# Kernel tuning notes

Hardware: AMD Instinct MI355X
Metric: run time of the kernel (lower is better)

The kernel has to match this reference:

```python
import jax, jax.numpy as jnp
import numpy as np

N = 50000   # nodes
E = 800000  # edges (avg degree 16)
IN, H, OUT = 128, 128, 64


def setup_inputs() -> dict:
    key = jax.random.key(0)
    ks = jax.random.split(key, 8)

    def w(k, shape):
        fan_in = shape[0]
        return (jax.random.normal(k, shape, jnp.float32) / np.float32(np.sqrt(fan_in)))

    x = jax.random.normal(ks[0], (N, IN), jnp.float32)
    edge_index = jax.random.randint(ks[1], (2, E), 0, N, jnp.int64)
    return {
        "x": x,
        "edge_index": edge_index,
        "W1": w(ks[2], (IN, H)), "b1": jnp.zeros((H,), jnp.float32),
        "W2": w(ks[3], (H, H)),  "b2": jnp.zeros((H,), jnp.float32),
        "W3": w(ks[4], (H, H)),  "b3": jnp.zeros((H,), jnp.float32),
        "Wd1": w(ks[5], (H, H)), "bd1": jnp.zeros((H,), jnp.float32),
        "Wd2": w(ks[6], (H, OUT)), "bd2": jnp.zeros((OUT,), jnp.float32),
    }


def _gcn_conv(x, src, dst, norm, W, b):
    # x: [N, Cin] -> linear transform, gather along edges, normalized scatter-add
    h = x @ W                                   # [N, Cout]
    msg = h[src] * norm[:, None]                # [E+N, Cout]
    out = jax.ops.segment_sum(msg, dst, num_segments=N)
    return out + b


def reference(x, edge_index, W1, b1, W2, b2, W3, b3, Wd1, bd1, Wd2, bd2):
    # Add self-loops (PyG GCNConv default) and compute symmetric normalization.
    loops = jnp.arange(N, dtype=edge_index.dtype)
    src = jnp.concatenate([edge_index[0], loops])   # [E+N]
    dst = jnp.concatenate([edge_index[1], loops])   # [E+N]
    deg = jax.ops.segment_sum(jnp.ones_like(dst, dtype=x.dtype), dst, num_segments=N)
    dinv = jnp.where(deg > 0, jax.lax.rsqrt(deg), jnp.zeros_like(deg))
    norm = dinv[src] * dinv[dst]                    # [E+N]

    h = jax.nn.relu(_gcn_conv(x, src, dst, norm, W1, b1))
    h = jax.nn.relu(_gcn_conv(h, src, dst, norm, W2, b2))
    h = jax.nn.relu(_gcn_conv(h, src, dst, norm, W3, b3))

    h = jax.nn.relu(h @ Wd1 + bd1)
    return jax.nn.sigmoid(h @ Wd2 + bd2)            # [N, OUT]
```

## Files before the change

kernel.cpp:

```cpp
#include <hip/hip_runtime.h>
#include <hip/hip_bf16.h>
#include <hip/hip_fp16.h>

#define N_NODES 50000
#define N_EDGES 800000
#define C_H 128
#define C_OUT 64
#define NBLK 196
#define TSTRIDE 136
#define E_PAD 1200128
#define MM_BLKS 782
#define TILE_N 6250
#define GB 782

typedef __attribute__((ext_vector_type(8))) short bf16x8;
typedef __attribute__((ext_vector_type(4))) float f32x4;

static __device__ __forceinline__ float bf_lo(unsigned int u) { return __uint_as_float(u << 16); }
static __device__ __forceinline__ float bf_hi(unsigned int u) { return __uint_as_float(u & 0xffff0000u); }
static __device__ __forceinline__ unsigned short f2bf(float f) {
    __hip_bfloat16 h = __float2bfloat16(f);
    return *(unsigned short*)&h;
}
static __device__ __forceinline__ unsigned int pack2(float a, float b) {
    return (unsigned int)f2bf(a) | ((unsigned int)f2bf(b) << 16);
}
static __device__ __forceinline__ unsigned short f2h_bits(float f) {
    union { __half h; unsigned short u; } c; c.h = __float2half_rn(f); return c.u;
}
static __device__ __forceinline__ float h_bits2f(unsigned short u) {
    union { __half h; unsigned short u; } c; c.u = u; return __half2float(c.h);
}

__global__ void prep_kernel(const int* __restrict__ src, const int* __restrict__ dst,
                            int* __restrict__ counts2,
                            int* __restrict__ rank,
                            const float* __restrict__ W1, const float* __restrict__ W2,
                            const float* __restrict__ W3, const float* __restrict__ Wd1,
                            const float* __restrict__ Wd2,
                            unsigned short* __restrict__ P1, unsigned short* __restrict__ P2,
                            unsigned short* __restrict__ P3, unsigned short* __restrict__ Pd1,
                            unsigned short* __restrict__ Pd2,
                            unsigned int* __restrict__ epay) {
    int b = blockIdx.x;
    if (b < 3125) {
        int e = b * 256 + threadIdx.x;
        int d = dst[e], s = src[e];
        int t = s / TILE_N;
        rank[e] = atomicAdd(&counts2[d * 8 + t], 1);
    } else if (b < 3413) {
        int idx = (b - 3125) * 256 + threadIdx.x;
        if (idx < 4 * 16384) {
            int which = idx >> 14;
            int r = idx & 16383;
            const float* W = (which == 0) ? W1 : (which == 1) ? W2 : (which == 2) ? W3 : Wd1;
            unsigned short* P = (which == 0) ? P1 : (which == 1) ? P2 : (which == 2) ? P3 : Pd1;
            int j = r & 7, lane = (r >> 3) & 63, t = r >> 9;
            int nb = t & 7, kb = t >> 3;
            int k = kb * 32 + ((lane >> 4) << 3) + j;
            int n = nb * 16 + (lane & 15);
            P[r] = f2bf(W[(size_t)k * 128 + n]);
        } else {
            int r = idx - 65536;
            if (r < 8192) {
                int j = r & 7, lane = (r >> 3) & 63, t = r >> 9;
                int nb = t & 3, kb = t >> 2;
                int k = kb * 32 + ((lane >> 4) << 3) + j;
                int n = nb * 16 + (lane & 15);
                Pd2[r] = f2bf(Wd2[(size_t)k * 64 + n]);
            }
        }
    } else {
        int i = (b - 3413) * 256 + threadIdx.x;
        *(uint4*)(epay + (size_t)i * 4) = make_uint4(0, 0, 0, 0);
    }
}

__global__ void __launch_bounds__(256) scan1_kernel(int* __restrict__ counts2,
                                                    int* __restrict__ eblk,
                                                    int* __restrict__ bsum,
                                                    float* __restrict__ dinv) {
    __shared__ int ws[4];
    int i = blockIdx.x * 256 + threadIdx.x;
    int vp = 0;
    if (i < N_NODES) {
        int* c = counts2 + (size_t)i * 8;
        uint4 a = *(uint4*)c;
        uint4 bq = *(uint4*)(c + 4);
        int raw = a.x + a.y + a.z + a.w + bq.x + bq.y + bq.z + bq.w;
        dinv[i] = rsqrtf((float)raw + 1.0f);
        int run = 0, tv;
        tv = ((int)a.x + 1) & ~1;  a.x  = run; run += tv;
        tv = ((int)a.y + 1) & ~1;  a.y  = run; run += tv;
        tv = ((int)a.z + 1) & ~1;  a.z  = run; run += tv;
        tv = ((int)a.w + 1) & ~1;  a.w  = run; run += tv;
        tv = ((int)bq.x + 1) & ~1; bq.x = run; run += tv;
        tv = ((int)bq.y + 1) & ~1; bq.y = run; run += tv;
        tv = ((int)bq.z + 1) & ~1; bq.z = run; run += tv;
        tv = ((int)bq.w + 1) & ~1; bq.w = run; run += tv;
        vp = run;
        *(uint4*)c = a;
        *(uint4*)(c + 4) = bq;
    }
    int lane = threadIdx.x & 63, w = threadIdx.x >> 6;
    int x = vp;
    #pragma unroll
    for (int off = 1; off < 64; off <<= 1) {
        int t = __shfl_up(x, off, 64);
        if (lane >= off) x += t;
    }
    if (lane == 63) ws[w] = x;
    __syncthreads();
    if (threadIdx.x == 0) {
        int run = 0;
        #pragma unroll
        for (int k = 0; k < 4; ++k) { int t = ws[k]; ws[k] = run; run += t; }
        bsum[blockIdx.x] = run;
    }
    __syncthreads();
    if (i < N_NODES) eblk[i] = x - vp + ws[w];
}

__global__ void __launch_bounds__(256) scanB_kernel(const int* __restrict__ eblk,
                                                    const int* __restrict__ bsum,
                                                    int* __restrict__ rowptr) {
    __shared__ int ws[4];
    __shared__ int sbo;
    int i = threadIdx.x;
    int v = (i < NBLK) ? bsum[i] : 0;
    int lane = i & 63, w = i >> 6;
    int x = v;
    #pragma unroll
    for (int off = 1; off < 64; off <<= 1) {
        int t = __shfl_up(x, off, 64);
        if (lane >= off) x += t;
    }
    if (lane == 63) ws[w] = x;
    __syncthreads();
    if (i == 0) {
        int run = 0;
        #pragma unroll
        for (int k = 0; k < 4; ++k) { int t = ws[k]; ws[k] = run; run += t; }
    }
    __syncthreads();
    int excl = x - v + ws[w];
    if (i == (int)blockIdx.x) sbo = excl;
    if (blockIdx.x == 0 && i == NBLK - 1) rowptr[N_NODES] = excl + v;
    __syncthreads();
    int g = blockIdx.x * 256 + threadIdx.x;
    if (g < N_NODES) rowptr[g] = eblk[g] + sbo;
}

__global__ void __launch_bounds__(256) fill_mm_kernel(
        const float* __restrict__ x, const unsigned short* __restrict__ P1,
        unsigned short* __restrict__ XW1,
        const int* __restrict__ src, const int* __restrict__ dst,
        const float* __restrict__ dinv,
        const int* __restrict__ rowptr, const int* __restrict__ counts2,
        const int* __restrict__ rank,
        unsigned int* __restrict__ epay) {
    int b = blockIdx.x;
    if (b < MM_BLKS) {
        const int lane = threadIdx.x & 63;
        const int wave = threadIdx.x >> 6;
        const int wid  = b * 4 + wave;
        if (wid * 16 >= N_NODES) return;
        const int node = wid * 16 + (lane & 15);
        const int quad = lane >> 4;
        f32x4 acc[8];
        #pragma unroll
        for (int nb = 0; nb < 8; ++nb) acc[nb] = (f32x4){0.f, 0.f, 0.f, 0.f};
        #pragma unroll
        for (int kb = 0; kb < 4; ++kb) {
            const float* p = x + (size_t)node * 128 + kb * 32 + quad * 8;
            float4 lo = *(const float4*)p;
            float4 hi = *(const float4*)(p + 4);
            union { bf16x8 v; unsigned int u[4]; } tmp;
            tmp.u[0] = pack2(lo.x, lo.y); tmp.u[1] = pack2(lo.z, lo.w);
            tmp.u[2] = pack2(hi.x, hi.y); tmp.u[3] = pack2(hi.z, hi.w);
            #pragma unroll
            for (int nb = 0; nb < 8; ++nb) {
                bf16x8 wf = *(const bf16x8*)(P1 + ((size_t)(kb * 8 + nb) * 64 + lane) * 8);
                acc[nb] = __builtin_amdgcn_mfma_f32_16x16x32_bf16(wf, tmp.v, acc[nb], 0, 0, 0);
            }
        }
        #pragma unroll
        for (int nb = 0; nb < 8; ++nb) {
            int ch = nb * 16 + quad * 4;
            uint2 o;
            o.x = pack2(acc[nb][0], acc[nb][1]);
            o.y = pack2(acc[nb][2], acc[nb][3]);
            *(uint2*)(XW1 + (size_t)node * C_H + ch) = o;
        }
    } else {
        int e = (b - MM_BLKS) * 256 + threadIdx.x;
        if (e < N_EDGES) {
            int d = dst[e], s = src[e];
            int t = s / TILE_N;
            int pos = rowptr[d] + counts2[d * 8 + t] + rank[e];
            float nrm = dinv[s] * dinv[d];
            epay[pos] = (unsigned int)s | ((unsigned int)f2h_bits(nrm) << 16);
        }
    }
}

static __device__ __forceinline__ void fma8v(float* a, uint4 q, float nm) {
    a[0] = fmaf(bf_lo(q.x), nm, a[0]); a[1] = fmaf(bf_hi(q.x), nm, a[1]);
    a[2] = fmaf(bf_lo(q.y), nm, a[2]); a[3] = fmaf(bf_hi(q.y), nm, a[3]);
    a[4] = fmaf(bf_lo(q.z), nm, a[4]); a[5] = fmaf(bf_hi(q.z), nm, a[5]);
    a[6] = fmaf(bf_lo(q.w), nm, a[6]); a[7] = fmaf(bf_hi(q.w), nm, a[7]);
}

static __device__ __forceinline__ void agg32(
        const int* __restrict__ rowptr, const int* __restrict__ counts2,
        const unsigned int* __restrict__ epay,
        const unsigned short* __restrict__ hin,
        const float* __restrict__ dinv,
        int node, int cb, float* acc) {
    const unsigned short* hc = hin + cb;
    float di = dinv[node], dii = di * di;
    {
        const unsigned short* rp = hc + (size_t)node * C_H;
        uint4 q0 = *(const uint4*)rp,        q1 = *(const uint4*)(rp + 8);
        uint4 q2 = *(const uint4*)(rp + 16), q3 = *(const uint4*)(rp + 24);
        fma8v(acc + 0, q0, dii); fma8v(acc + 8, q1, dii);
        fma8v(acc + 16, q2, dii); fma8v(acc + 24, q3, dii);
    }
    int base = rowptr[node];
    int rend = rowptr[node + 1];
    const int* boff = counts2 + (size_t)node * 8;
    #pragma unroll 1
    for (int t = 0; t < 8; ++t) {
        int b0 = base + boff[t];
        int b1 = (t == 7) ? rend : base + boff[t + 1];
        for (int p = b0; p < b1; p += 2) {
            uint2 ev = *(const uint2*)(epay + p);
            const unsigned short* ra = hc + (size_t)(ev.x & 0xffffu) * C_H;
            const unsigned short* rb = hc + (size_t)(ev.y & 0xffffu) * C_H;
            uint4 a0 = *(const uint4*)ra,        a1 = *(const uint4*)(ra + 8);
            uint4 a2 = *(const uint4*)(ra + 16), a3 = *(const uint4*)(ra + 24);
            uint4 c0 = *(const uint4*)rb,        c1 = *(const uint4*)(rb + 8);
            uint4 c2 = *(const uint4*)(rb + 16), c3 = *(const uint4*)(rb + 24);
            float na = h_bits2f((unsigned short)(ev.x >> 16));
            float nb = h_bits2f((unsigned short)(ev.y >> 16));
            fma8v(acc + 0, a0, na); fma8v(acc + 8, a1, na);
            fma8v(acc + 16, a2, na); fma8v(acc + 24, a3, na);
            fma8v(acc + 0, c0, nb); fma8v(acc + 8, c1, nb);
            fma8v(acc + 16, c2, nb); fma8v(acc + 24, c3, nb);
        }
    }
}

__global__ void __launch_bounds__(256, 4) gather1_kernel(
        const int* __restrict__ rowptr, const int* __restrict__ counts2,
        const unsigned int* __restrict__ epay,
        const float* __restrict__ dinv,
        const unsigned short* __restrict__ hin,
        const float* __restrict__ bias,
        unsigned short* __restrict__ out) {
    const int t = threadIdx.x;
    const int node = blockIdx.x * 64 + (t >> 2);
    if (node >= N_NODES) return;
    const int cb = (t & 3) << 5;

    float acc[32];
    #pragma unroll
    for (int j = 0; j < 32; ++j) acc[j] = 0.f;
    agg32(rowptr, counts2, epay, hin, dinv, node, cb, acc);

    #pragma unroll
    for (int g = 0; g < 4; ++g) {
        float4 ba = *(const float4*)(bias + cb + g * 8);
        float4 bb = *(const float4*)(bias + cb + g * 8 + 4);
        float v0 = fmaxf(acc[g*8+0] + ba.x, 0.f), v1 = fmaxf(acc[g*8+1] + ba.y, 0.f);
        float v2 = fmaxf(acc[g*8+2] + ba.z, 0.f), v3 = fmaxf(acc[g*8+3] + ba.w, 0.f);
        float v4 = fmaxf(acc[g*8+4] + bb.x, 0.f), v5 = fmaxf(acc[g*8+5] + bb.y, 0.f);
        float v6 = fmaxf(acc[g*8+6] + bb.z, 0.f), v7 = fmaxf(acc[g*8+7] + bb.w, 0.f);
        uint4 o;
        o.x = pack2(v0, v1); o.y = pack2(v2, v3);
        o.z = pack2(v4, v5); o.w = pack2(v6, v7);
        *(uint4*)(out + (size_t)node * C_H + cb + g * 8) = o;
    }
}

template <bool FINAL>
__global__ void __launch_bounds__(256, 4) fused_layer_kernel(
        const int* __restrict__ rowptr, const int* __restrict__ counts2,
        const unsigned int* __restrict__ epay,
        const float* __restrict__ dinv,
        const unsigned short* __restrict__ hin,
        const unsigned short* __restrict__ Wp,
        const float* __restrict__ bias,
        const unsigned short* __restrict__ Wd1p,
        const float* __restrict__ bd1,
        const unsigned short* __restrict__ Wd2p,
        const float* __restrict__ bd2,
        unsigned short* __restrict__ out_b,
        float* __restrict__ out_f) {
    __shared__ unsigned short sA[64 * TSTRIDE];
    __shared__ unsigned short sB[64 * TSTRIDE];
    const int t = threadIdx.x;

    {
        const int ln = t >> 2;
        const int node = blockIdx.x * 64 + ln;
        const int cb = (t & 3) << 5;
        float acc[32];
        #pragma unroll
        for (int j = 0; j < 32; ++j) acc[j] = 0.f;
        if (node < N_NODES)
            agg32(rowptr, counts2, epay, hin, dinv, node, cb, acc);
        #pragma unroll
        for (int g = 0; g < 4; ++g) {
            uint4 o;
            o.x = pack2(acc[g*8+0], acc[g*8+1]); o.y = pack2(acc[g*8+2], acc[g*8+3]);
            o.z = pack2(acc[g*8+4], acc[g*8+5]); o.w = pack2(acc[g*8+6], acc[g*8+7]);
            *(uint4*)(sA + ln * TSTRIDE + cb + g * 8) = o;
        }
    }
    __syncthreads();

    const int lane = t & 63, wave = t >> 6, quad = lane >> 4, row = lane & 15;
    const int nb0 = 2 * wave, nb1 = 2 * wave + 1;

    #pragma unroll 1
    for (int rt = 0; rt < 4; ++rt) {
        const int lrow = rt * 16 + row;
        const int node = blockIdx.x * 64 + lrow;
        f32x4 acc0 = (f32x4){0.f, 0.f, 0.f, 0.f};
        f32x4 acc1 = (f32x4){0.f, 0.f, 0.f, 0.f};
        #pragma unroll
        for (int kb = 0; kb < 4; ++kb) {
            bf16x8 hf = *(const bf16x8*)(sA + lrow * TSTRIDE + kb * 32 + quad * 8);
            bf16x8 wf0 = *(const bf16x8*)(Wp + ((size_t)(kb * 8 + nb0) * 64 + lane) * 8);
            bf16x8 wf1 = *(const bf16x8*)(Wp + ((size_t)(kb * 8 + nb1) * 64 + lane) * 8);
            acc0 = __builtin_amdgcn_mfma_f32_16x16x32_bf16(wf0, hf, acc0, 0, 0, 0);
            acc1 = __builtin_amdgcn_mfma_f32_16x16x32_bf16(wf1, hf, acc1, 0, 0, 0);
        }
        float4 ba0 = *(const float4*)(bias + nb0 * 16 + quad * 4);
        float4 ba1 = *(const float4*)(bias + nb1 * 16 + quad * 4);
        float v00 = fmaxf(acc0[0] + ba0.x, 0.f), v01 = fmaxf(acc0[1] + ba0.y, 0.f);
        float v02 = fmaxf(acc0[2] + ba0.z, 0.f), v03 = fmaxf(acc0[3] + ba0.w, 0.f);
        float v10 = fmaxf(acc1[0] + ba1.x, 0.f), v11 = fmaxf(acc1[1] + ba1.y, 0.f);
        float v12 = fmaxf(acc1[2] + ba1.z, 0.f), v13 = fmaxf(acc1[3] + ba1.w, 0.f);
        uint2 o0, o1;
        o0.x = pack2(v00, v01); o0.y = pack2(v02, v03);
        o1.x = pack2(v10, v11); o1.y = pack2(v12, v13);
        if (!FINAL) {
            if (node < N_NODES) {
                *(uint2*)(out_b + (size_t)node * C_H + nb0 * 16 + quad * 4) = o0;
                *(uint2*)(out_b + (size_t)node * C_H + nb1 * 16 + quad * 4) = o1;
            }
        } else {
            *(uint2*)(sB + lrow * TSTRIDE + nb0 * 16 + quad * 4) = o0;
            *(uint2*)(sB + lrow * TSTRIDE + nb1 * 16 + quad * 4) = o1;
        }
    }
    if (!FINAL) return;

    __syncthreads();
    #pragma unroll 1
    for (int rt = 0; rt < 4; ++rt) {
        const int lrow = rt * 16 + row;
        f32x4 acc0 = (f32x4){0.f, 0.f, 0.f, 0.f};
        f32x4 acc1 = (f32x4){0.f, 0.f, 0.f, 0.f};
        #pragma unroll
        for (int kb = 0; kb < 4; ++kb) {
            bf16x8 hf = *(const bf16x8*)(sB + lrow * TSTRIDE + kb * 32 + quad * 8);
            bf16x8 wf0 = *(const bf16x8*)(Wd1p + ((size_t)(kb * 8 + nb0) * 64 + lane) * 8);
            bf16x8 wf1 = *(const bf16x8*)(Wd1p + ((size_t)(kb * 8 + nb1) * 64 + lane) * 8);
            acc0 = __builtin_amdgcn_mfma_f32_16x16x32_bf16(wf0, hf, acc0, 0, 0, 0);
            acc1 = __builtin_amdgcn_mfma_f32_16x16x32_bf16(wf1, hf, acc1, 0, 0, 0);
        }
        float4 ba0 = *(const float4*)(bd1 + nb0 * 16 + quad * 4);
        float4 ba1 = *(const float4*)(bd1 + nb1 * 16 + quad * 4);
        float v00 = fmaxf(acc0[0] + ba0.x, 0.f), v01 = fmaxf(acc0[1] + ba0.y, 0.f);
        float v02 = fmaxf(acc0[2] + ba0.z, 0.f), v03 = fmaxf(acc0[3] + ba0.w, 0.f);
        float v10 = fmaxf(acc1[0] + ba1.x, 0.f), v11 = fmaxf(acc1[1] + ba1.y, 0.f);
        float v12 = fmaxf(acc1[2] + ba1.z, 0.f), v13 = fmaxf(acc1[3] + ba1.w, 0.f);
        uint2 o0, o1;
        o0.x = pack2(v00, v01); o0.y = pack2(v02, v03);
        o1.x = pack2(v10, v11); o1.y = pack2(v12, v13);
        *(uint2*)(sA + lrow * TSTRIDE + nb0 * 16 + quad * 4) = o0;
        *(uint2*)(sA + lrow * TSTRIDE + nb1 * 16 + quad * 4) = o1;
    }
    __syncthreads();

    #pragma unroll 1
    for (int rt = 0; rt < 4; ++rt) {
        const int lrow = rt * 16 + row;
        const int node = blockIdx.x * 64 + lrow;
        f32x4 acc = (f32x4){0.f, 0.f, 0.f, 0.f};
        #pragma unroll
        for (int kb = 0; kb < 4; ++kb) {
            bf16x8 hf = *(const bf16x8*)(sA + lrow * TSTRIDE + kb * 32 + quad * 8);
            bf16x8 wf = *(const bf16x8*)(Wd2p + ((size_t)(kb * 4 + wave) * 64 + lane) * 8);
            acc = __builtin_amdgcn_mfma_f32_16x16x32_bf16(wf, hf, acc, 0, 0, 0);
        }
        if (node < N_NODES) {
            int ch = wave * 16 + quad * 4;
            float4 b4 = *(const float4*)(bd2 + ch);
            float4 rr;
            rr.x = 1.f / (1.f + expf(-(acc[0] + b4.x)));
            rr.y = 1.f / (1.f + expf(-(acc[1] + b4.y)));
            rr.z = 1.f / (1.f + expf(-(acc[2] + b4.z)));
            rr.w = 1.f / (1.f + expf(-(acc[3] + b4.w)));
            *(float4*)(out_f + (size_t)node * C_OUT + ch) = rr;
        }
    }
}

extern "C" void kernel_launch(void* const* d_in, const int* in_sizes, int n_in,
                              void* d_out, int out_size, void* d_ws, size_t ws_size,
                              hipStream_t stream) {
    const float* x   = (const float*)d_in[0];
    const int*   ei  = (const int*)d_in[1];
    const float* W1  = (const float*)d_in[2];
    const float* b1  = (const float*)d_in[3];
    const float* W2  = (const float*)d_in[4];
    const float* b2  = (const float*)d_in[5];
    const float* W3  = (const float*)d_in[6];
    const float* b3  = (const float*)d_in[7];
    const float* Wd1 = (const float*)d_in[8];
    const float* bd1 = (const float*)d_in[9];
    const float* Wd2 = (const float*)d_in[10];
    const float* bd2 = (const float*)d_in[11];

    const int* src = ei;
    const int* dst = ei + N_EDGES;

    char* base = (char*)d_ws;
    size_t off = 0;
    auto alloc = [&](size_t bytes) { char* p = base + off; off += (bytes + 255) & ~size_t(255); return p; };
    int*            counts2 = (int*)alloc((size_t)N_NODES * 8 * 4);
    unsigned int*   epay   = (unsigned int*)alloc((size_t)E_PAD * 4);
    int*            rank   = (int*)alloc((size_t)N_EDGES * 4);
    float*          dinv   = (float*)alloc(N_NODES * 4);
    int*            rowptr = (int*)alloc((N_NODES + 1) * 4);
    int*            eblk   = (int*)alloc(N_NODES * 4);
    int*            bsum   = (int*)alloc(256 * 4);
    unsigned short* XW1    = (unsigned short*)alloc((size_t)N_NODES * C_H * 2);
    unsigned short* bufA   = (unsigned short*)alloc((size_t)N_NODES * C_H * 2);
    unsigned short* bufB   = (unsigned short*)alloc((size_t)N_NODES * C_H * 2);
    unsigned short* P1     = (unsigned short*)alloc(128 * 128 * 2);
    unsigned short* P2     = (unsigned short*)alloc(128 * 128 * 2);
    unsigned short* P3     = (unsigned short*)alloc(128 * 128 * 2);
    unsigned short* Pd1    = (unsigned short*)alloc(128 * 128 * 2);
    unsigned short* Pd2    = (unsigned short*)alloc(128 * 64 * 2);

    const int T = 256;
    dim3 blk(T);
    dim3 gN((N_NODES + T - 1) / T);
    dim3 gPrep(3125 + 288 + 1172);
    dim3 gFillMM(MM_BLKS + 3125);
    dim3 gGB(GB);

    hipMemsetAsync(counts2, 0, (size_t)N_NODES * 8 * 4, stream);
    prep_kernel<<<gPrep, blk, 0, stream>>>(src, dst, counts2, rank,
                                           W1, W2, W3, Wd1, Wd2,
                                           P1, P2, P3, Pd1, Pd2, epay);
    scan1_kernel<<<gN, blk, 0, stream>>>(counts2, eblk, bsum, dinv);
    scanB_kernel<<<gN, blk, 0, stream>>>(eblk, bsum, rowptr);
    fill_mm_kernel<<<gFillMM, blk, 0, stream>>>(x, P1, XW1, src, dst, dinv,
                                                rowptr, counts2, rank, epay);

    gather1_kernel<<<gGB, blk, 0, stream>>>(rowptr, counts2, epay, dinv, XW1, b1, bufA);
    fused_layer_kernel<false><<<gGB, blk, 0, stream>>>(
        rowptr, counts2, epay, dinv, bufA, P2, b2, nullptr, nullptr, nullptr, nullptr, bufB, nullptr);
    fused_layer_kernel<true><<<gGB, blk, 0, stream>>>(
        rowptr, counts2, epay, dinv, bufB, P3, b3, Pd1, bd1, Pd2, bd2, nullptr, (float*)d_out);
}
```

Measured before the change: 293.9 us.

## Use wave-per-16-nodes gather with each lane owning two channels

Changes the edge aggregation from four threads per node, each holding 32 channels, to one wavefront per 16 nodes where each lane holds two channels of a node row. Each gathered neighbor row becomes a single coalesced 256-byte wave access instead of per-thread 64-byte strided loads, and per-thread register use for accumulators shrinks. In exchange the 16 nodes of a wave are walked one after another, so edge-index loads become wave-uniform and serialized. Nodes with different degrees are processed sequentially inside the wave, and each edge now brings less work per load, which may lower memory-level parallelism.

```diff
diff --git a/kernel.cpp b/kernel.cpp
--- a/kernel.cpp
+++ b/kernel.cpp
@@ -204,49 +204,41 @@
     }
 }
 
-static __device__ __forceinline__ void fma8v(float* a, uint4 q, float nm) {
-    a[0] = fmaf(bf_lo(q.x), nm, a[0]); a[1] = fmaf(bf_hi(q.x), nm, a[1]);
-    a[2] = fmaf(bf_lo(q.y), nm, a[2]); a[3] = fmaf(bf_hi(q.y), nm, a[3]);
-    a[4] = fmaf(bf_lo(q.z), nm, a[4]); a[5] = fmaf(bf_hi(q.z), nm, a[5]);
-    a[6] = fmaf(bf_lo(q.w), nm, a[6]); a[7] = fmaf(bf_hi(q.w), nm, a[7]);
-}
-
-static __device__ __forceinline__ void agg32(
+static __device__ __forceinline__ void wave_gather16(
         const int* __restrict__ rowptr, const int* __restrict__ counts2,
         const unsigned int* __restrict__ epay,
+        const float* __restrict__ dinv,
         const unsigned short* __restrict__ hin,
-        const float* __restrict__ dinv,
-        int node, int cb, float* acc) {
-    const unsigned short* hc = hin + cb;
-    float di = dinv[node], dii = di * di;
-    {
-        const unsigned short* rp = hc + (size_t)node * C_H;
-        uint4 q0 = *(const uint4*)rp,        q1 = *(const uint4*)(rp + 8);
-        uint4 q2 = *(const uint4*)(rp + 16), q3 = *(const uint4*)(rp + 24);
-        fma8v(acc + 0, q0, dii); fma8v(acc + 8, q1, dii);
-        fma8v(acc + 16, q2, dii); fma8v(acc + 24, q3, dii);
-    }
-    int base = rowptr[node];
-    int rend = rowptr[node + 1];
-    const int* boff = counts2 + (size_t)node * 8;
+        int nbase, int lane2, float* accA, float* accB) {
+    int rbase[16];
+    #pragma unroll
+    for (int nn = 0; nn < 16; ++nn) {
+        int node = nbase + nn; if (node >= N_NODES) node = N_NODES - 1;
+        float di = dinv[node], dii = di * di;
+        unsigned int rw = *(const unsigned int*)(hin + (size_t)node * C_H + lane2);
+        accA[nn] = bf_lo(rw) * dii;
+        accB[nn] = bf_hi(rw) * dii;
+        rbase[nn] = rowptr[node];
+    }
     #pragma unroll 1
     for (int t = 0; t < 8; ++t) {
-        int b0 = base + boff[t];
-        int b1 = (t == 7) ? rend : base + boff[t + 1];
-        for (int p = b0; p < b1; p += 2) {
-            uint2 ev = *(const uint2*)(epay + p);
-            const unsigned short* ra = hc + (size_t)(ev.x & 0xffffu) * C_H;
-            const unsigned short* rb = hc + (size_t)(ev.y & 0xffffu) * C_H;
-            uint4 a0 = *(const uint4*)ra,        a1 = *(const uint4*)(ra + 8);
-            uint4 a2 = *(const uint4*)(ra + 16), a3 = *(const uint4*)(ra + 24);
-            uint4 c0 = *(const uint4*)rb,        c1 = *(const uint4*)(rb + 8);
-            uint4 c2 = *(const uint4*)(rb + 16), c3 = *(const uint4*)(rb + 24);
-            float na = h_bits2f((unsigned short)(ev.x >> 16));
-            float nb = h_bits2f((unsigned short)(ev.y >> 16));
-            fma8v(acc + 0, a0, na); fma8v(acc + 8, a1, na);
-            fma8v(acc + 16, a2, na); fma8v(acc + 24, a3, na);
-            fma8v(acc + 0, c0, nb); fma8v(acc + 8, c1, nb);
-            fma8v(acc + 16, c2, nb); fma8v(acc + 24, c3, nb);
+        #pragma unroll
+        for (int nn = 0; nn < 16; ++nn) {
+            int node = nbase + nn; if (node >= N_NODES) node = N_NODES - 1;
+            const int* c2 = counts2 + (size_t)node * 8;
+            int b0 = rbase[nn] + c2[t];
+            int b1 = (t < 7) ? rbase[nn] + c2[t + 1] : rowptr[node + 1];
+            float a = accA[nn], b = accB[nn];
+            for (int p = b0; p < b1; p += 2) {
+                uint2 ev = *(const uint2*)(epay + p);
+                unsigned int ra = *(const unsigned int*)(hin + (size_t)(ev.x & 0xffffu) * C_H + lane2);
+                unsigned int rb = *(const unsigned int*)(hin + (size_t)(ev.y & 0xffffu) * C_H + lane2);
+                float na = h_bits2f((unsigned short)(ev.x >> 16));
+                float nb = h_bits2f((unsigned short)(ev.y >> 16));
+                a = fmaf(bf_lo(ra), na, a); b = fmaf(bf_hi(ra), na, b);
+                a = fmaf(bf_lo(rb), nb, a); b = fmaf(bf_hi(rb), nb, b);
+            }
+            accA[nn] = a; accB[nn] = b;
         }
     }
 }
@@ -259,27 +251,22 @@
         const float* __restrict__ bias,
         unsigned short* __restrict__ out) {
     const int t = threadIdx.x;
-    const int node = blockIdx.x * 64 + (t >> 2);
-    if (node >= N_NODES) return;
-    const int cb = (t & 3) << 5;
-
-    float acc[32];
+    const int lane = t & 63, wave = t >> 6;
+    const int lane2 = lane * 2;
+    const int nbase = blockIdx.x * 64 + wave * 16;
+
+    float accA[16], accB[16];
+    wave_gather16(rowptr, counts2, epay, dinv, hin, nbase, lane2, accA, accB);
+
+    float b0 = bias[lane2], b1 = bias[lane2 + 1];
     #pragma unroll
-    for (int j = 0; j < 32; ++j) acc[j] = 0.f;
-    agg32(rowptr, counts2, epay, hin, dinv, node, cb, acc);
-
-    #pragma unroll
-    for (int g = 0; g < 4; ++g) {
-        float4 ba = *(const float4*)(bias + cb + g * 8);
-        float4 bb = *(const float4*)(bias + cb + g * 8 + 4);
-        float v0 = fmaxf(acc[g*8+0] + ba.x, 0.f), v1 = fmaxf(acc[g*8+1] + ba.y, 0.f);
-        float v2 = fmaxf(acc[g*8+2] + ba.z, 0.f), v3 = fmaxf(acc[g*8+3] + ba.w, 0.f);
-        float v4 = fmaxf(acc[g*8+4] + bb.x, 0.f), v5 = fmaxf(acc[g*8+5] + bb.y, 0.f);
-        float v6 = fmaxf(acc[g*8+6] + bb.z, 0.f), v7 = fmaxf(acc[g*8+7] + bb.w, 0.f);
-        uint4 o;
-        o.x = pack2(v0, v1); o.y = pack2(v2, v3);
-        o.z = pack2(v4, v5); o.w = pack2(v6, v7);
-        *(uint4*)(out + (size_t)node * C_H + cb + g * 8) = o;
+    for (int nn = 0; nn < 16; ++nn) {
+        int node = nbase + nn;
+        if (node < N_NODES) {
+            float v0 = fmaxf(accA[nn] + b0, 0.f);
+            float v1 = fmaxf(accB[nn] + b1, 0.f);
+            *(unsigned int*)(out + (size_t)node * C_H + lane2) = pack2(v0, v1);
+        }
     }
 }
 
@@ -300,27 +287,22 @@
     __shared__ unsigned short sA[64 * TSTRIDE];
     __shared__ unsigned short sB[64 * TSTRIDE];
     const int t = threadIdx.x;
+    const int lane = t & 63, wave = t >> 6;
 
     {
-        const int ln = t >> 2;
-        const int node = blockIdx.x * 64 + ln;
-        const int cb = (t & 3) << 5;
-        float acc[32];
-        #pragma unroll
-        for (int j = 0; j < 32; ++j) acc[j] = 0.f;
-        if (node < N_NODES)
-            agg32(rowptr, counts2, epay, hin, dinv, node, cb, acc);
-        #pragma unroll
-        for (int g = 0; g < 4; ++g) {
-            uint4 o;
-            o.x = pack2(acc[g*8+0], acc[g*8+1]); o.y = pack2(acc[g*8+2], acc[g*8+3]);
-            o.z = pack2(acc[g*8+4], acc[g*8+5]); o.w = pack2(acc[g*8+6], acc[g*8+7]);
-            *(uint4*)(sA + ln * TSTRIDE + cb + g * 8) = o;
-        }
-    }
-    __syncthreads();
-
-    const int lane = t & 63, wave = t >> 6, quad = lane >> 4, row = lane & 15;
+        const int lane2 = lane * 2;
+        const int nbase = blockIdx.x * 64 + wave * 16;
+        float accA[16], accB[16];
+        wave_gather16(rowptr, counts2, epay, dinv, hin, nbase, lane2, accA, accB);
+        #pragma unroll
+        for (int nn = 0; nn < 16; ++nn) {
+            *(unsigned int*)(sA + (wave * 16 + nn) * TSTRIDE + lane2) =
+                pack2(accA[nn], accB[nn]);
+        }
+    }
+    __syncthreads();
+
+    const int quad = lane >> 4, row = lane & 15;
     const int nb0 = 2 * wave, nb1 = 2 * wave + 1;
 
     #pragma unroll 1
```

Result: slower. 574.9 us (+95.6%).
